# Kernel optimization log

Hardware: AMD Instinct MI355X
Metric: run time of the kernel (lower is better)

## Reference

```python
import jax, jax.numpy as jnp
import numpy as np

EPS = 1e-15


def _cdist(a, b):
    # batched euclidean pairwise distance, a:[B,N,K] b:[B,M,K] -> [B,N,M]
    d2 = (jnp.sum(a * a, -1)[:, :, None] + jnp.sum(b * b, -1)[:, None, :]
          - 2.0 * jnp.einsum('bik,bjk->bij', a, b))
    return jnp.sqrt(jnp.maximum(d2, 0.0))


def _rank3_diag(d_flat):
    # [B,N] -> [B,N,N] diagonal
    eye = jnp.eye(d_flat.shape[1], dtype=d_flat.dtype)
    return eye * d_flat[:, :, None]


def _trace(m):
    return jnp.einsum('bjj->b', m)


def dense_ct_rewiring(x, adj, s, mask):
    s = jnp.tanh(s)
    m = mask[:, :, None].astype(x.dtype)
    x = x * m
    s = s * m
    k = s.shape[-1]
    d_flat = jnp.sum(adj, axis=-1)              # [B,N]
    d = _rank3_diag(d_flat) + EPS               # EPS added to full matrix (faithful to torch)
    L = d - adj
    out_adj = jnp.einsum('bnk,bnm,bml->bkl', s, L, s)
    ct_num = _trace(out_adj)
    ct_den = _trace(jnp.einsum('bnk,bnm,bml->bkl', s, d, s)) + EPS
    ct_dist = _cdist(s, s)                      # [B,N,N]
    vol = _trace(d)                             # [B]
    ct_dist = ct_dist / vol[:, None, None]
    adj_new = ct_dist * adj
    ct_loss = jnp.mean(ct_num / ct_den)
    ss = jnp.einsum('bnk,bnl->bkl', s, s)
    i_s = jnp.eye(k, dtype=ss.dtype)
    ss_n = jnp.sqrt(jnp.sum(ss * ss, axis=(-1, -2), keepdims=True))
    diff = ss / ss_n - i_s
    ortho_loss = jnp.sqrt(jnp.sum(diff * diff))  # global Frobenius norm, mean of scalar
    return adj_new, ct_loss, ortho_loss


def dense_mincut_pool(x, adj, s, mask):
    s = jax.nn.softmax(s, axis=-1)
    m = mask[:, :, None].astype(x.dtype)
    x = x * m
    s = s * m
    k = s.shape[-1]
    out = jnp.einsum('bnk,bnf->bkf', s, x)
    out_adj = jnp.einsum('bnk,bnm,bml->bkl', s, adj, s)
    mincut_num = _trace(out_adj)
    d_flat = jnp.sum(adj, axis=-1) + EPS
    d = _rank3_diag(d_flat)
    mincut_den = _trace(jnp.einsum('bnk,bnm,bml->bkl', s, d, s))
    mincut_loss = jnp.mean(-(mincut_num / mincut_den))
    ss = jnp.einsum('bnk,bnl->bkl', s, s)
    i_s = jnp.eye(k, dtype=ss.dtype)
    ss_n = jnp.sqrt(jnp.sum(ss * ss, axis=(-1, -2), keepdims=True))
    diff = ss / ss_n - i_s / jnp.sqrt(jnp.asarray(float(k), ss.dtype))
    ortho_loss = jnp.mean(jnp.sqrt(jnp.sum(diff * diff, axis=(-1, -2))))
    # zero diagonal, then symmetric degree normalization
    out_adj = out_adj * (1.0 - i_s)
    dk = jnp.sqrt(jnp.sum(out_adj, axis=-1) + EPS) + EPS  # [B,k]
    out_adj = out_adj / dk[:, None, :] / dk[:, :, None]
    return out, out_adj, mincut_loss, ortho_loss


def dense_graph_conv(x, adj, w_rel, b_rel, w_root):
    # PyG DenseGraphConv(aggr='add'): lin_rel(adj @ x) + lin_root(x)
    return jnp.matmul(jnp.matmul(adj, x), w_rel) + b_rel + jnp.matmul(x, w_root)


def ctnet_forward(x, adj, mask,
                  W_lin1, b_lin1, W_pool1, b_pool1, W_pool2, b_pool2,
                  Wrel1, brel1, Wroot1, Wrel2, brel2, Wroot2,
                  W_lin2, b_lin2, W_lin3, b_lin3):
    x = jnp.matmul(x, W_lin1) + b_lin1
    s1 = jnp.matmul(x, W_pool1) + b_pool1
    adj, ct_loss, ortho1 = dense_ct_rewiring(x, adj, s1, mask)
    x = dense_graph_conv(x, adj, Wrel1, brel1, Wroot1)
    s2 = jnp.matmul(x, W_pool2) + b_pool2
    x, adj, mincut2, ortho2 = dense_mincut_pool(x, adj, s2, mask)
    x = dense_graph_conv(x, adj, Wrel2, brel2, Wroot2)
    x = jnp.sum(x, axis=1)
    x = jax.nn.relu(jnp.matmul(x, W_lin2) + b_lin2)
    x = jnp.matmul(x, W_lin3) + b_lin3
    return jax.nn.log_softmax(x, axis=-1), ct_loss + ortho1, mincut2 + ortho2


def _init_lin(key, fan_in, fan_out):
    k1, k2 = jax.random.split(key)
    lim = 1.0 / np.sqrt(fan_in)
    W = jax.random.uniform(k1, (fan_in, fan_out), jnp.float32, -lim, lim)
    b = jax.random.uniform(k2, (fan_out,), jnp.float32, -lim, lim)
    return W, b


def setup_inputs() -> dict:
    key = jax.random.key(0)
    ks = jax.random.split(key, 12)
    B, N, Fin, H, K, OUT, K2 = 16, 1024, 128, 32, 64, 10, 16
    x = jax.random.normal(ks[0], (B, N, Fin), jnp.float32)
    adj = jax.random.uniform(ks[1], (B, N, N), jnp.float32)
    mask = jnp.ones((B, N), jnp.bool_)
    W_lin1, b_lin1 = _init_lin(ks[2], Fin, H)
    W_pool1, b_pool1 = _init_lin(ks[3], H, K)
    W_pool2, b_pool2 = _init_lin(ks[4], H, K2)
    Wrel1, brel1 = _init_lin(ks[5], H, H)
    Wroot1, _ = _init_lin(ks[6], H, H)
    Wrel2, brel2 = _init_lin(ks[7], H, H)
    Wroot2, _ = _init_lin(ks[8], H, H)
    W_lin2, b_lin2 = _init_lin(ks[9], H, H)
    W_lin3, b_lin3 = _init_lin(ks[10], H, OUT)
    return dict(x=x, adj=adj, mask=mask,
                W_lin1=W_lin1, b_lin1=b_lin1, W_pool1=W_pool1, b_pool1=b_pool1,
                W_pool2=W_pool2, b_pool2=b_pool2,
                Wrel1=Wrel1, brel1=brel1, Wroot1=Wroot1,
                Wrel2=Wrel2, brel2=brel2, Wroot2=Wroot2,
                W_lin2=W_lin2, b_lin2=b_lin2, W_lin3=W_lin3, b_lin3=b_lin3)


def reference(x, adj, mask,
              W_lin1, b_lin1, W_pool1, b_pool1, W_pool2, b_pool2,
              Wrel1, brel1, Wroot1, Wrel2, brel2, Wroot2,
              W_lin2, b_lin2, W_lin3, b_lin3):
    return ctnet_forward(x, adj, mask,
                         W_lin1, b_lin1, W_pool1, b_pool1, W_pool2, b_pool2,
                         Wrel1, brel1, Wroot1, Wrel2, brel2, Wroot2,
                         W_lin2, b_lin2, W_lin3, b_lin3)
```

## Files before the change

### kernel.cpp

```cpp
#include <hip/hip_runtime.h>

typedef unsigned short u16;
typedef unsigned int   u32;
typedef __attribute__((ext_vector_type(8))) short bf16x8;
typedef __attribute__((ext_vector_type(4))) float f32x4;

#define EPSF 1e-15f

__device__ __forceinline__ float* accp(float* xb, int b, int a) {
    return xb + (size_t)(b*1024 + a/14)*128 + 114 + (a % 14);
}

__device__ __forceinline__ float bf2f(u16 u) {
    union { u32 i; float f; } v; v.i = ((u32)u) << 16; return v.f;
}
__device__ __forceinline__ u16 f2bf(float f) {
    union { u32 i; float f; } v; v.f = f;
    u32 r = v.i + 0x7fffu + ((v.i >> 16) & 1u);
    return (u16)(r >> 16);
}

__global__ __launch_bounds__(256) void k_a(float* xb,
        const float* __restrict__ W1, const float* __restrict__ b1,
        const float* __restrict__ Wp1, const float* __restrict__ bp1)
{
    __shared__ float W1s[128*32];
    __shared__ float Wp1s[32*64];
    __shared__ float xs[16][128];
    __shared__ float x1s[16][32];
    int tid = threadIdx.x;
    for (int i = tid; i < 1024; i += 256)
        *(float4*)&W1s[i*4] = *(const float4*)&W1[i*4];
    for (int i = tid; i < 512; i += 256)
        *(float4*)&Wp1s[i*4] = *(const float4*)&Wp1[i*4];
    int rbase = blockIdx.x*16;
    for (int e = tid; e < 512; e += 256) {
        int rr = e >> 5, c = e & 31;
        *(float4*)&xs[rr][c*4] = *(const float4*)&xb[(size_t)(rbase + rr)*128 + c*4];
    }
    __syncthreads();
    int w = tid >> 6, l = tid & 63;
    #pragma unroll
    for (int i = 0; i < 4; ++i) {
        int rr = w*4 + i;
        float* xr = xb + (size_t)(rbase + rr)*128;
        if (l < 32) xr[32 + l] = 0.f;
        if (l == 33) xr[96] = 0.f;
        if (l < 15) xr[113 + l] = 0.f;
        if (l < 32) {
            float acc = b1[l];
            for (int f = 0; f < 128; ++f) acc += xs[rr][f]*W1s[f*32 + l];
            x1s[rr][l] = acc;
        }
    }
    __syncthreads();
    #pragma unroll
    for (int i = 0; i < 4; ++i) {
        int rr = w*4 + i;
        float* xr = xb + (size_t)(rbase + rr)*128;
        if (l < 32) xr[64 + l] = x1s[rr][l];
        float acc = bp1[l];
        for (int h = 0; h < 32; ++h) acc += x1s[rr][h]*Wp1s[h*64 + l];
        float sv = tanhf(acc);
        u32 me = (u32)f2bf(sv);
        u32 nb = __shfl_down(me, 1);
        if (!(l & 1)) ((u32*)xr)[l >> 1] = me | (nb << 16);
        float svr = bf2f((u16)me);
        float qv = svr*svr;
        for (int off = 32; off; off >>= 1) qv += __shfl_down(qv, off);
        if (l == 0) xr[112] = qv;
    }
}

__global__ __launch_bounds__(256, 6) void k_c(const float* __restrict__ adj, float* xb,
                                              u32* __restrict__ anb)
{
    __shared__ __align__(16) u16 BufA[64*72];
    __shared__ __align__(16) u16 BufB[64*72];
    __shared__ __align__(16) float qAs[64], qBs[64];
    __shared__ float pw[2][4];
    int tid = threadIdx.x;
    int tj = blockIdx.x, ti = blockIdx.y, b = blockIdx.z;
    int w = tid >> 6, lane = tid & 63;
    int q = lane >> 4, c16 = lane & 15;
    int rloc = w*16 + c16;
    size_t rowg = (size_t)(b*1024 + ti*64 + rloc);
    float4 a4s[4];
    #pragma unroll
    for (int t = 0; t < 4; ++t)
        a4s[t] = *(const float4*)&adj[rowg*1024 + tj*64 + t*16 + q*4];
    const u32* xu = (const u32*)xb;
    for (int e = tid; e < 512; e += 256) {
        int n = e >> 3, c = e & 7;
        *(float4*)&BufA[n*72 + c*8] = *(const float4*)&xu[(size_t)(b*1024 + ti*64 + n)*128 + c*4];
    }
    for (int e = tid; e < 512; e += 256) {
        int n = e >> 3, c = e & 7;
        *(float4*)&BufB[n*72 + c*8] = *(const float4*)&xu[(size_t)(b*1024 + tj*64 + n)*128 + c*4];
    }
    if (tid < 64) qAs[tid] = xb[(size_t)(b*1024 + ti*64 + tid)*128 + 112];
    else if (tid < 128) qBs[tid - 64] = xb[(size_t)(b*1024 + tj*64 + (tid - 64))*128 + 112];
    __syncthreads();
    bf16x8 bfr0 = *(const bf16x8*)&BufA[rloc*72 + q*8];
    bf16x8 bfr1 = *(const bf16x8*)&BufA[rloc*72 + 32 + q*8];
    float qa = qAs[rloc];
    f32x4 g[4];
    #pragma unroll
    for (int t = 0; t < 4; ++t) {
        bf16x8 af0 = *(const bf16x8*)&BufB[(t*16 + c16)*72 + q*8];
        bf16x8 af1 = *(const bf16x8*)&BufB[(t*16 + c16)*72 + 32 + q*8];
        f32x4 gg = {0.f, 0.f, 0.f, 0.f};
        gg = __builtin_amdgcn_mfma_f32_16x16x32_bf16(af0, bfr0, gg, 0, 0, 0);
        gg = __builtin_amdgcn_mfma_f32_16x16x32_bf16(af1, bfr1, gg, 0, 0, 0);
        g[t] = gg;
    }
    float dsum = 0.f, rsum = 0.f, Pt = 0.f, Qt = 0.f;
    #pragma unroll
    for (int t = 0; t < 4; ++t) {
        float4 a4 = a4s[t];
        float4 qb4 = *(const float4*)&qBs[t*16 + q*4];
        float av[4] = {a4.x, a4.y, a4.z, a4.w};
        float qb[4] = {qb4.x, qb4.y, qb4.z, qb4.w};
        float o[4];
        #pragma unroll
        for (int rg = 0; rg < 4; ++rg) {
            float d2v = qa + qb[rg] - 2.f*g[t][rg];
            float dist = sqrtf(fmaxf(d2v, 0.f));
            o[rg] = dist * av[rg];
            dsum += av[rg];
            rsum += o[rg];
            Pt += av[rg]*g[t][rg];
            Qt += g[t][rg]*g[t][rg];
        }
        u32 p0 = (u32)f2bf(o[0]) | ((u32)f2bf(o[1]) << 16);
        u32 p1 = (u32)f2bf(o[2]) | ((u32)f2bf(o[3]) << 16);
        *(uint2*)&anb[rowg*512 + tj*32 + t*8 + q*2] = make_uint2(p0, p1);
    }
    rsum += __shfl_xor(rsum, 16); rsum += __shfl_xor(rsum, 32);
    dsum += __shfl_xor(dsum, 16); dsum += __shfl_xor(dsum, 32);
    if (q == 0) {
        atomicAdd(&xb[rowg*128 + 96],  dsum);
        atomicAdd(&xb[rowg*128 + 113], rsum);
    }
    for (int off = 32; off; off >>= 1) { Pt += __shfl_down(Pt, off); Qt += __shfl_down(Qt, off); }
    if (lane == 0) { pw[0][w] = Pt; pw[1][w] = Qt; }
    __syncthreads();
    if (tid == 0) {
        atomicAdd(accp(xb,b,3), pw[0][0]+pw[0][1]+pw[0][2]+pw[0][3]);
        atomicAdd(accp(xb,b,4), pw[1][0]+pw[1][1]+pw[1][2]+pw[1][3]);
    }
}

__global__ __launch_bounds__(256) void k_y(const u32* __restrict__ anb, float* xb)
{
    __shared__ __align__(16) u16 X[32][264];
    int tid = threadIdx.x;
    int kq = blockIdx.x, ni = blockIdx.y, b = blockIdx.z;
    int w = tid >> 6, lane = tid & 63;
    int q = lane >> 4, c16 = lane & 15;
    int rloc = w*16 + c16;
    size_t rowg = (size_t)(b*1024 + ni*64 + rloc);
    bf16x8 afv[8];
    #pragma unroll
    for (int ks = 0; ks < 8; ++ks)
        afv[ks] = *(const bf16x8*)&anb[rowg*512 + kq*128 + ks*16 + q*4];
    for (int e = tid; e < 2048; e += 256) {
        int m = e >> 3, hq = e & 7;
        const float4 v = *(const float4*)&xb[(size_t)(b*1024 + kq*256 + m)*128 + 64 + hq*4];
        X[hq*4 + 0][m] = f2bf(v.x);
        X[hq*4 + 1][m] = f2bf(v.y);
        X[hq*4 + 2][m] = f2bf(v.z);
        X[hq*4 + 3][m] = f2bf(v.w);
    }
    __syncthreads();
    f32x4 acc0 = {0.f,0.f,0.f,0.f}, acc1 = {0.f,0.f,0.f,0.f};
    #pragma unroll
    for (int ks = 0; ks < 8; ++ks) {
        bf16x8 b0 = *(const bf16x8*)&X[c16][ks*32 + q*8];
        bf16x8 b1v = *(const bf16x8*)&X[c16 + 16][ks*32 + q*8];
        acc0 = __builtin_amdgcn_mfma_f32_16x16x32_bf16(afv[ks], b0,  acc0, 0, 0, 0);
        acc1 = __builtin_amdgcn_mfma_f32_16x16x32_bf16(afv[ks], b1v, acc1, 0, 0, 0);
    }
    #pragma unroll
    for (int rg = 0; rg < 4; ++rg) {
        size_t orow = (size_t)(b*1024 + ni*64 + w*16 + q*4 + rg)*128;
        atomicAdd(&xb[orow + 32 + c16], acc0[rg]);
        atomicAdd(&xb[orow + 48 + c16], acc1[rg]);
    }
    if (kq == 0 && tid < 64) {
        const float* xr = xb + (size_t)(b*1024 + ni*64 + tid)*128;
        float d = xr[96], qv = xr[112];
        float t0 = d, t1 = d*qv, t2 = qv;
        for (int off = 32; off; off >>= 1) {
            t0 += __shfl_down(t0, off); t1 += __shfl_down(t1, off); t2 += __shfl_down(t2, off);
        }
        if (tid == 0) {
            atomicAdd(accp(xb,b,0), t0);
            atomicAdd(accp(xb,b,1), t1);
            atomicAdd(accp(xb,b,2), t2);
        }
    }
}

__global__ __launch_bounds__(256) void k_d2(float* xb,
        const float* __restrict__ Wrel1, const float* __restrict__ brel1,
        const float* __restrict__ Wroot1,
        const float* __restrict__ Wp2, const float* __restrict__ bp2)
{
    __shared__ float ys[32*34];
    __shared__ float x1n[32*34];
    __shared__ float x2s[32*34];
    __shared__ float s2s[32*17];
    __shared__ float Wr[1024], Wo[1024], Wp[512];
    int tid = threadIdx.x;
    int tq = blockIdx.x, b = blockIdx.y;
    int rbase = b*1024 + tq*32;
    float invv = 1.f / (*accp(xb,b,0) + 1024.f*EPSF);
    for (int i = tid; i < 1024; i += 256) { Wr[i] = Wrel1[i]; Wo[i] = Wroot1[i]; }
    for (int i = tid; i < 512; i += 256) Wp[i] = Wp2[i];
    for (int e = tid; e < 1024; e += 256) {
        int r = e >> 5, h = e & 31;
        const float* xr = xb + (size_t)(rbase + r)*128;
        ys[r*34 + h]  = xr[32 + h] * invv;
        x1n[r*34 + h] = xr[64 + h];
    }
    __syncthreads();
    {
        int h = tid & 31, tg = tid >> 5;
        float brl = brel1[h];
        #pragma unroll
        for (int i = 0; i < 4; ++i) {
            int r = tg + 8*i;
            float v = brl;
            for (int j = 0; j < 32; ++j)
                v += ys[r*34 + j]*Wr[j*32 + h] + x1n[r*34 + j]*Wo[j*32 + h];
            x2s[r*34 + h] = v;
        }
    }
    __syncthreads();
    if (tid < 64) {
        int r = tid & 31;
        float lg[16];
        float mx = -1e30f;
        #pragma unroll
        for (int k = 0; k < 16; ++k) {
            float v = bp2[k];
            for (int j = 0; j < 32; ++j) v += x2s[r*34 + j]*Wp[j*16 + k];
            lg[k] = v; mx = fmaxf(mx, v);
        }
        float sum = 0.f;
        #pragma unroll
        for (int k = 0; k < 16; ++k) { lg[k] = expf(lg[k] - mx); sum += lg[k]; }
        float inv = 1.f/sum, q2v = 0.f;
        u32 pk[8];
        #pragma unroll
        for (int k = 0; k < 16; ++k) {
            float sv = lg[k]*inv;
            s2s[r*17 + k] = sv;
            u32 bfv = (u32)f2bf(sv);
            if (k & 1) pk[k>>1] |= bfv << 16; else pk[k>>1] = bfv;
            q2v += sv*sv;
        }
        if (tid < 32) {
            u32* xp = (u32*)(xb + (size_t)(rbase + r)*128);
            #pragma unroll
            for (int i2 = 0; i2 < 8; ++i2) xp[i2] = pk[i2];
        }
        float denp = (xb[(size_t)(rbase + r)*128 + 113]*invv + EPSF)*q2v;
        if (tid >= 32) denp = 0.f;
        for (int off = 32; off; off >>= 1) denp += __shfl_down(denp, off);
        if (tid == 0) atomicAdd(accp(xb,b,5), denp);
    }
    __syncthreads();
    {
        int k = tid >> 4, l = tid & 15;
        float s = 0.f;
        for (int r = 0; r < 32; ++r) s += s2s[r*17 + k]*s2s[r*17 + l];
        atomicAdd(accp(xb,b,774 + tid), s);
    }
    for (int e = tid; e < 512; e += 256) {
        int k = e >> 5, h = e & 31;
        float s = 0.f;
        for (int r = 0; r < 32; ++r) s += s2s[r*17 + k]*x2s[r*34 + h];
        atomicAdd(accp(xb,b,6 + k*32 + h), s);
    }
}

__global__ __launch_bounds__(256, 6) void k_e(const u32* __restrict__ anb, float* xb)
{
    __shared__ __align__(16) u16 BufA[64*72];
    __shared__ __align__(16) u16 BufS[16*72];
    __shared__ __align__(16) u16 BufN[16*72];
    __shared__ __align__(16) u16 zT[16*72];
    int tid = threadIdx.x;
    int miq = blockIdx.x, ni = blockIdx.y, b = blockIdx.z;
    const u32* xu = (const u32*)xb;
    for (int e = tid; e < 512; e += 256) {
        int node = e >> 3, lw = e & 7;
        u32 pp = xu[(size_t)(b*1024 + ni*64 + node)*128 + lw];
        BufN[(lw*2)*72 + node]     = (u16)pp;
        BufN[(lw*2 + 1)*72 + node] = (u16)(pp >> 16);
    }
    int w = tid >> 6, lane = tid & 63;
    int q = lane >> 4, c16 = lane & 15;
    int rloc = w*16 + c16;
    f32x4 zacc = {0.f, 0.f, 0.f, 0.f};
    #pragma unroll
    for (int mii = 0; mii < 2; ++mii) {
        int mi = miq*2 + mii;
        __syncthreads();
        for (int e = tid; e < 512; e += 256) {
            int n = e >> 3, c = e & 7;
            *(float4*)&BufA[n*72 + c*8] =
                *(const float4*)&anb[(size_t)(b*1024 + ni*64 + n)*512 + mi*32 + c*4];
        }
        for (int e = tid; e < 512; e += 256) {
            int node = e >> 3, lw = e & 7;
            u32 pp = xu[(size_t)(b*1024 + mi*64 + node)*128 + lw];
            BufS[(lw*2)*72 + node]     = (u16)pp;
            BufS[(lw*2 + 1)*72 + node] = (u16)(pp >> 16);
        }
        __syncthreads();
        bf16x8 ya0 = *(const bf16x8*)&BufA[rloc*72 + q*8];
        bf16x8 ya1 = *(const bf16x8*)&BufA[rloc*72 + 32 + q*8];
        bf16x8 yb0 = *(const bf16x8*)&BufS[c16*72 + q*8];
        bf16x8 yb1 = *(const bf16x8*)&BufS[c16*72 + 32 + q*8];
        zacc = __builtin_amdgcn_mfma_f32_16x16x32_bf16(ya0, yb0, zacc, 0, 0, 0);
        zacc = __builtin_amdgcn_mfma_f32_16x16x32_bf16(ya1, yb1, zacc, 0, 0, 0);
    }
    #pragma unroll
    for (int rg = 0; rg < 4; ++rg)
        zT[c16*72 + w*16 + q*4 + rg] = f2bf(zacc[rg]);
    __syncthreads();
    if (w == 0) {
        bf16x8 af0 = *(const bf16x8*)&BufN[c16*72 + q*8];
        bf16x8 af1 = *(const bf16x8*)&BufN[c16*72 + 32 + q*8];
        bf16x8 bz0 = *(const bf16x8*)&zT[c16*72 + q*8];
        bf16x8 bz1 = *(const bf16x8*)&zT[c16*72 + 32 + q*8];
        f32x4 oamv = {0.f, 0.f, 0.f, 0.f};
        oamv = __builtin_amdgcn_mfma_f32_16x16x32_bf16(af0, bz0, oamv, 0, 0, 0);
        oamv = __builtin_amdgcn_mfma_f32_16x16x32_bf16(af1, bz1, oamv, 0, 0, 0);
        #pragma unroll
        for (int rg = 0; rg < 4; ++rg)
            atomicAdd(accp(xb, b, 518 + (q*4 + rg)*16 + c16), oamv[rg]);
    }
}

__global__ __launch_bounds__(256) void k_f1(float* xb,
        const float* __restrict__ Wrel2, const float* __restrict__ brel2,
        const float* __restrict__ Wroot2,
        const float* __restrict__ W_lin2, const float* __restrict__ b_lin2,
        const float* __restrict__ W_lin3, const float* __restrict__ b_lin3,
        float* __restrict__ outp)
{
    __shared__ float oam_s[256], ssm_s[256], outm_s[512];
    __shared__ float dks[16], csoa[16];
    __shared__ float cs0[32], cs1[32], xsum[32], x5[32], lgs[10];
    __shared__ float red[4];
    int b = blockIdx.x;
    int tid = threadIdx.x;
    float invv = 1.f / (*accp(xb,b,0) + 1024.f*EPSF);
    oam_s[tid] = *accp(xb,b,518 + tid) * invv;
    ssm_s[tid] = *accp(xb,b,774 + tid);
    for (int e = tid; e < 512; e += 256) outm_s[e] = *accp(xb,b,6 + e);
    __syncthreads();
    if (tid < 16) {
        float rsv = 0.f;
        for (int l = 0; l < 16; ++l) if (l != tid) rsv += oam_s[tid*16 + l];
        dks[tid] = sqrtf(fmaxf(rsv, 0.f) + EPSF) + EPSF;
    }
    {
        float v = ssm_s[tid];
        float p = v*v;
        for (int off = 32; off; off >>= 1) p += __shfl_down(p, off);
        if ((tid & 63) == 0) red[tid >> 6] = p;
    }
    __syncthreads();
    if (tid < 16) {
        float s = 0.f;
        for (int k2 = 0; k2 < 16; ++k2)
            if (k2 != tid) s += oam_s[k2*16 + tid] / dks[k2];
        csoa[tid] = s / dks[tid];
    }
    if (tid < 32) {
        float s0 = 0.f, s1 = 0.f;
        for (int l = 0; l < 16; ++l) {
            float ov = outm_s[l*32 + tid];
            s0 += ov;
            s1 += csoa[l] * ov;
        }
        cs0[tid] = s0; cs1[tid] = s1;
    }
    if (tid == 64) {
        float T1v  = *accp(xb,b,1);
        float Pgv  = *accp(xb,b,3);
        float Q2v  = *accp(xb,b,4);
        float Tq1v = *accp(xb,b,2);
        float T2v  = *accp(xb,b,5);
        *accp(xb,b,1030) = (T1v - Pgv) / (T1v + EPSF);
        *accp(xb,b,1031) = 65.f - 2.f*Tq1v/sqrtf(fmaxf(Q2v, 1e-30f));
        float tr2 = 0.f, trs = 0.f;
        for (int k2 = 0; k2 < 16; ++k2) { tr2 += oam_s[k2*17]; trs += ssm_s[k2*17]; }
        *accp(xb,b,1032) = -tr2 / T2v;
        float fr2 = red[0] + red[1] + red[2] + red[3];
        *accp(xb,b,1033) = sqrtf(fmaxf(2.f - trs/(2.f*sqrtf(fmaxf(fr2, 1e-30f))), 0.f));
    }
    __syncthreads();
    if (tid < 32) {
        float v = 16.f * brel2[tid];
        for (int j = 0; j < 32; ++j)
            v += cs1[j]*Wrel2[j*32 + tid] + cs0[j]*Wroot2[j*32 + tid];
        xsum[tid] = v;
    }
    __syncthreads();
    if (tid < 32) {
        float v = b_lin2[tid];
        for (int j = 0; j < 32; ++j) v += xsum[j]*W_lin2[j*32 + tid];
        x5[tid] = fmaxf(v, 0.f);
    }
    __syncthreads();
    if (tid < 10) {
        float v = b_lin3[tid];
        for (int j = 0; j < 32; ++j) v += x5[j]*W_lin3[j*10 + tid];
        lgs[tid] = v;
    }
    __syncthreads();
    if (tid < 10) {
        float mx = -1e30f;
        for (int t = 0; t < 10; ++t) mx = fmaxf(mx, lgs[t]);
        float sum = 0.f;
        for (int t = 0; t < 10; ++t) sum += expf(lgs[t] - mx);
        outp[b*10 + tid] = lgs[tid] - mx - logf(sum);
    }
}

__global__ __launch_bounds__(64) void k_f2(float* xb, float* __restrict__ outp)
{
    int tid = threadIdx.x;
    int b2 = tid & 15, which = tid >> 4;
    float v = *accp(xb, b2, 1030 + which);
    for (int off = 1; off < 16; off <<= 1) v += __shfl_xor(v, off);
    float ct = __shfl(v, 0);
    float o1 = __shfl(v, 16);
    float mc = __shfl(v, 32);
    float o2 = __shfl(v, 48);
    if (tid == 0) {
        outp[160] = ct/16.f + sqrtf(fmaxf(o1, 0.f));
        outp[161] = mc/16.f + o2/16.f;
    }
}

extern "C" void kernel_launch(void* const* d_in, const int* in_sizes, int n_in,
                              void* d_out, int out_size, void* d_ws, size_t ws_size,
                              hipStream_t stream)
{
    float* xb        = (float*)d_in[0];
    const float* adj = (const float*)d_in[1];
    const float* W_lin1 = (const float*)d_in[3];
    const float* b_lin1 = (const float*)d_in[4];
    const float* W_pool1= (const float*)d_in[5];
    const float* b_pool1= (const float*)d_in[6];
    const float* W_pool2= (const float*)d_in[7];
    const float* b_pool2= (const float*)d_in[8];
    const float* Wrel1  = (const float*)d_in[9];
    const float* brel1  = (const float*)d_in[10];
    const float* Wroot1 = (const float*)d_in[11];
    const float* Wrel2  = (const float*)d_in[12];
    const float* brel2  = (const float*)d_in[13];
    const float* Wroot2 = (const float*)d_in[14];
    const float* W_lin2 = (const float*)d_in[15];
    const float* b_lin2 = (const float*)d_in[16];
    const float* W_lin3 = (const float*)d_in[17];
    const float* b_lin3 = (const float*)d_in[18];
    u32* anb = (u32*)d_ws;
    (void)ws_size; (void)in_sizes; (void)n_in; (void)out_size;

    k_a<<<dim3(1024),      dim3(256), 0, stream>>>(xb, W_lin1, b_lin1, W_pool1, b_pool1);
    k_c<<<dim3(16,16,16),  dim3(256), 0, stream>>>(adj, xb, anb);
    k_y<<<dim3(4,16,16),   dim3(256), 0, stream>>>(anb, xb);
    k_d2<<<dim3(32,16),    dim3(256), 0, stream>>>(xb, Wrel1, brel1, Wroot1,
                                                   W_pool2, b_pool2);
    k_e<<<dim3(8,16,16),   dim3(256), 0, stream>>>(anb, xb);
    k_f1<<<dim3(16),       dim3(256), 0, stream>>>(xb, Wrel2, brel2, Wroot2,
                                                   W_lin2, b_lin2, W_lin3, b_lin3,
                                                   (float*)d_out);
    k_f2<<<dim3(1),        dim3(64),  0, stream>>>(xb, (float*)d_out);
}
```

Before: 247.1 us.

## Widen adjacency tiles, drop split-K atomics in k_y, fold final reduction into k_f1

Result: faster. 227.5 us (-7.9%).

```diff
diff --git a/kernel.cpp b/kernel.cpp
--- a/kernel.cpp
+++ b/kernel.cpp
@@ -40,18 +40,19 @@
     }
     __syncthreads();
     int w = tid >> 6, l = tid & 63;
+    int col = l & 31, half = l >> 5;
     #pragma unroll
     for (int i = 0; i < 4; ++i) {
         int rr = w*4 + i;
         float* xr = xb + (size_t)(rbase + rr)*128;
-        if (l < 32) xr[32 + l] = 0.f;
         if (l == 33) xr[96] = 0.f;
         if (l < 15) xr[113 + l] = 0.f;
-        if (l < 32) {
-            float acc = b1[l];
-            for (int f = 0; f < 128; ++f) acc += xs[rr][f]*W1s[f*32 + l];
-            x1s[rr][l] = acc;
-        }
+        float acc = half ? 0.f : b1[col];
+        const float* xrow = &xs[rr][half*64];
+        const float* wrow = &W1s[half*64*32 + col];
+        for (int f = 0; f < 64; ++f) acc += xrow[f]*wrow[f*32];
+        acc += __shfl_down(acc, 32);
+        if (l < 32) x1s[rr][l] = acc;
     }
     __syncthreads();
     #pragma unroll
@@ -72,69 +73,80 @@
     }
 }
 
-__global__ __launch_bounds__(256, 6) void k_c(const float* __restrict__ adj, float* xb,
+__global__ __launch_bounds__(256, 5) void k_c(const float* __restrict__ adj, float* xb,
                                               u32* __restrict__ anb)
 {
     __shared__ __align__(16) u16 BufA[64*72];
-    __shared__ __align__(16) u16 BufB[64*72];
-    __shared__ __align__(16) float qAs[64], qBs[64];
+    __shared__ __align__(16) u16 BufB[2][64*72];
+    __shared__ __align__(16) float qAs[64], qBs[2][64];
     __shared__ float pw[2][4];
     int tid = threadIdx.x;
-    int tj = blockIdx.x, ti = blockIdx.y, b = blockIdx.z;
+    int tjq = blockIdx.x, ti = blockIdx.y, b = blockIdx.z;
     int w = tid >> 6, lane = tid & 63;
     int q = lane >> 4, c16 = lane & 15;
     int rloc = w*16 + c16;
     size_t rowg = (size_t)(b*1024 + ti*64 + rloc);
-    float4 a4s[4];
-    #pragma unroll
-    for (int t = 0; t < 4; ++t)
-        a4s[t] = *(const float4*)&adj[rowg*1024 + tj*64 + t*16 + q*4];
+    float4 a4s[2][4];
+    #pragma unroll
+    for (int tt = 0; tt < 2; ++tt)
+        #pragma unroll
+        for (int t = 0; t < 4; ++t)
+            a4s[tt][t] = *(const float4*)&adj[rowg*1024 + (tjq*2 + tt)*64 + t*16 + q*4];
     const u32* xu = (const u32*)xb;
     for (int e = tid; e < 512; e += 256) {
         int n = e >> 3, c = e & 7;
         *(float4*)&BufA[n*72 + c*8] = *(const float4*)&xu[(size_t)(b*1024 + ti*64 + n)*128 + c*4];
     }
-    for (int e = tid; e < 512; e += 256) {
-        int n = e >> 3, c = e & 7;
-        *(float4*)&BufB[n*72 + c*8] = *(const float4*)&xu[(size_t)(b*1024 + tj*64 + n)*128 + c*4];
+    for (int e = tid; e < 1024; e += 256) {
+        int n2 = e >> 3, c = e & 7;
+        int tt = n2 >> 6, n = n2 & 63;
+        *(float4*)&BufB[tt][n*72 + c*8] =
+            *(const float4*)&xu[(size_t)(b*1024 + (tjq*2 + tt)*64 + n)*128 + c*4];
     }
     if (tid < 64) qAs[tid] = xb[(size_t)(b*1024 + ti*64 + tid)*128 + 112];
-    else if (tid < 128) qBs[tid - 64] = xb[(size_t)(b*1024 + tj*64 + (tid - 64))*128 + 112];
+    else if (tid < 192) {
+        int t2 = tid - 64;
+        qBs[t2 >> 6][t2 & 63] =
+            xb[(size_t)(b*1024 + (tjq*2 + (t2 >> 6))*64 + (t2 & 63))*128 + 112];
+    }
     __syncthreads();
     bf16x8 bfr0 = *(const bf16x8*)&BufA[rloc*72 + q*8];
     bf16x8 bfr1 = *(const bf16x8*)&BufA[rloc*72 + 32 + q*8];
     float qa = qAs[rloc];
-    f32x4 g[4];
-    #pragma unroll
-    for (int t = 0; t < 4; ++t) {
-        bf16x8 af0 = *(const bf16x8*)&BufB[(t*16 + c16)*72 + q*8];
-        bf16x8 af1 = *(const bf16x8*)&BufB[(t*16 + c16)*72 + 32 + q*8];
-        f32x4 gg = {0.f, 0.f, 0.f, 0.f};
-        gg = __builtin_amdgcn_mfma_f32_16x16x32_bf16(af0, bfr0, gg, 0, 0, 0);
-        gg = __builtin_amdgcn_mfma_f32_16x16x32_bf16(af1, bfr1, gg, 0, 0, 0);
-        g[t] = gg;
-    }
     float dsum = 0.f, rsum = 0.f, Pt = 0.f, Qt = 0.f;
     #pragma unroll
-    for (int t = 0; t < 4; ++t) {
-        float4 a4 = a4s[t];
-        float4 qb4 = *(const float4*)&qBs[t*16 + q*4];
-        float av[4] = {a4.x, a4.y, a4.z, a4.w};
-        float qb[4] = {qb4.x, qb4.y, qb4.z, qb4.w};
-        float o[4];
-        #pragma unroll
-        for (int rg = 0; rg < 4; ++rg) {
-            float d2v = qa + qb[rg] - 2.f*g[t][rg];
-            float dist = sqrtf(fmaxf(d2v, 0.f));
-            o[rg] = dist * av[rg];
-            dsum += av[rg];
-            rsum += o[rg];
-            Pt += av[rg]*g[t][rg];
-            Qt += g[t][rg]*g[t][rg];
-        }
-        u32 p0 = (u32)f2bf(o[0]) | ((u32)f2bf(o[1]) << 16);
-        u32 p1 = (u32)f2bf(o[2]) | ((u32)f2bf(o[3]) << 16);
-        *(uint2*)&anb[rowg*512 + tj*32 + t*8 + q*2] = make_uint2(p0, p1);
+    for (int tt = 0; tt < 2; ++tt) {
+        f32x4 g[4];
+        #pragma unroll
+        for (int t = 0; t < 4; ++t) {
+            bf16x8 af0 = *(const bf16x8*)&BufB[tt][(t*16 + c16)*72 + q*8];
+            bf16x8 af1 = *(const bf16x8*)&BufB[tt][(t*16 + c16)*72 + 32 + q*8];
+            f32x4 gg = {0.f, 0.f, 0.f, 0.f};
+            gg = __builtin_amdgcn_mfma_f32_16x16x32_bf16(af0, bfr0, gg, 0, 0, 0);
+            gg = __builtin_amdgcn_mfma_f32_16x16x32_bf16(af1, bfr1, gg, 0, 0, 0);
+            g[t] = gg;
+        }
+        #pragma unroll
+        for (int t = 0; t < 4; ++t) {
+            float4 a4 = a4s[tt][t];
+            float4 qb4 = *(const float4*)&qBs[tt][t*16 + q*4];
+            float av[4] = {a4.x, a4.y, a4.z, a4.w};
+            float qb[4] = {qb4.x, qb4.y, qb4.z, qb4.w};
+            float o[4];
+            #pragma unroll
+            for (int rg = 0; rg < 4; ++rg) {
+                float d2v = qa + qb[rg] - 2.f*g[t][rg];
+                float dist = sqrtf(fmaxf(d2v, 0.f));
+                o[rg] = dist * av[rg];
+                dsum += av[rg];
+                rsum += o[rg];
+                Pt += av[rg]*g[t][rg];
+                Qt += g[t][rg]*g[t][rg];
+            }
+            u32 p0 = (u32)f2bf(o[0]) | ((u32)f2bf(o[1]) << 16);
+            u32 p1 = (u32)f2bf(o[2]) | ((u32)f2bf(o[3]) << 16);
+            *(uint2*)&anb[rowg*512 + (tjq*2 + tt)*32 + t*8 + q*2] = make_uint2(p0, p1);
+        }
     }
     rsum += __shfl_xor(rsum, 16); rsum += __shfl_xor(rsum, 32);
     dsum += __shfl_xor(dsum, 16); dsum += __shfl_xor(dsum, 32);
@@ -153,20 +165,16 @@
 
 __global__ __launch_bounds__(256) void k_y(const u32* __restrict__ anb, float* xb)
 {
-    __shared__ __align__(16) u16 X[32][264];
+    __shared__ __align__(16) u16 X[32][1032];
     int tid = threadIdx.x;
-    int kq = blockIdx.x, ni = blockIdx.y, b = blockIdx.z;
+    int ni = blockIdx.x, b = blockIdx.y;
     int w = tid >> 6, lane = tid & 63;
     int q = lane >> 4, c16 = lane & 15;
     int rloc = w*16 + c16;
     size_t rowg = (size_t)(b*1024 + ni*64 + rloc);
-    bf16x8 afv[8];
-    #pragma unroll
-    for (int ks = 0; ks < 8; ++ks)
-        afv[ks] = *(const bf16x8*)&anb[rowg*512 + kq*128 + ks*16 + q*4];
-    for (int e = tid; e < 2048; e += 256) {
+    for (int e = tid; e < 8192; e += 256) {
         int m = e >> 3, hq = e & 7;
-        const float4 v = *(const float4*)&xb[(size_t)(b*1024 + kq*256 + m)*128 + 64 + hq*4];
+        const float4 v = *(const float4*)&xb[(size_t)(b*1024 + m)*128 + 64 + hq*4];
         X[hq*4 + 0][m] = f2bf(v.x);
         X[hq*4 + 1][m] = f2bf(v.y);
         X[hq*4 + 2][m] = f2bf(v.z);
@@ -174,20 +182,21 @@
     }
     __syncthreads();
     f32x4 acc0 = {0.f,0.f,0.f,0.f}, acc1 = {0.f,0.f,0.f,0.f};
-    #pragma unroll
-    for (int ks = 0; ks < 8; ++ks) {
-        bf16x8 b0 = *(const bf16x8*)&X[c16][ks*32 + q*8];
+    #pragma unroll 8
+    for (int ks = 0; ks < 32; ++ks) {
+        bf16x8 af  = *(const bf16x8*)&anb[rowg*512 + ks*16 + q*4];
+        bf16x8 b0  = *(const bf16x8*)&X[c16][ks*32 + q*8];
         bf16x8 b1v = *(const bf16x8*)&X[c16 + 16][ks*32 + q*8];
-        acc0 = __builtin_amdgcn_mfma_f32_16x16x32_bf16(afv[ks], b0,  acc0, 0, 0, 0);
-        acc1 = __builtin_amdgcn_mfma_f32_16x16x32_bf16(afv[ks], b1v, acc1, 0, 0, 0);
+        acc0 = __builtin_amdgcn_mfma_f32_16x16x32_bf16(af, b0,  acc0, 0, 0, 0);
+        acc1 = __builtin_amdgcn_mfma_f32_16x16x32_bf16(af, b1v, acc1, 0, 0, 0);
     }
     #pragma unroll
     for (int rg = 0; rg < 4; ++rg) {
         size_t orow = (size_t)(b*1024 + ni*64 + w*16 + q*4 + rg)*128;
-        atomicAdd(&xb[orow + 32 + c16], acc0[rg]);
-        atomicAdd(&xb[orow + 48 + c16], acc1[rg]);
-    }
-    if (kq == 0 && tid < 64) {
+        xb[orow + 32 + c16] = acc0[rg];
+        xb[orow + 48 + c16] = acc1[rg];
+    }
+    if (tid < 64) {
         const float* xr = xb + (size_t)(b*1024 + ni*64 + tid)*128;
         float d = xr[96], qv = xr[112];
         float t0 = d, t1 = d*qv, t2 = qv;
@@ -357,6 +366,7 @@
     __shared__ float dks[16], csoa[16];
     __shared__ float cs0[32], cs1[32], xsum[32], x5[32], lgs[10];
     __shared__ float red[4];
+    __shared__ int isLast;
     int b = blockIdx.x;
     int tid = threadIdx.x;
     float invv = 1.f / (*accp(xb,b,0) + 1024.f*EPSF);
@@ -397,13 +407,18 @@
         float Q2v  = *accp(xb,b,4);
         float Tq1v = *accp(xb,b,2);
         float T2v  = *accp(xb,b,5);
-        *accp(xb,b,1030) = (T1v - Pgv) / (T1v + EPSF);
-        *accp(xb,b,1031) = 65.f - 2.f*Tq1v/sqrtf(fmaxf(Q2v, 1e-30f));
         float tr2 = 0.f, trs = 0.f;
         for (int k2 = 0; k2 < 16; ++k2) { tr2 += oam_s[k2*17]; trs += ssm_s[k2*17]; }
-        *accp(xb,b,1032) = -tr2 / T2v;
         float fr2 = red[0] + red[1] + red[2] + red[3];
-        *accp(xb,b,1033) = sqrtf(fmaxf(2.f - trs/(2.f*sqrtf(fmaxf(fr2, 1e-30f))), 0.f));
+        __hip_atomic_store(accp(xb,b,1030), (T1v - Pgv) / (T1v + EPSF),
+                           __ATOMIC_RELAXED, __HIP_MEMORY_SCOPE_AGENT);
+        __hip_atomic_store(accp(xb,b,1031), 65.f - 2.f*Tq1v/sqrtf(fmaxf(Q2v, 1e-30f)),
+                           __ATOMIC_RELAXED, __HIP_MEMORY_SCOPE_AGENT);
+        __hip_atomic_store(accp(xb,b,1032), -tr2 / T2v,
+                           __ATOMIC_RELAXED, __HIP_MEMORY_SCOPE_AGENT);
+        __hip_atomic_store(accp(xb,b,1033),
+                           sqrtf(fmaxf(2.f - trs/(2.f*sqrtf(fmaxf(fr2, 1e-30f))), 0.f)),
+                           __ATOMIC_RELAXED, __HIP_MEMORY_SCOPE_AGENT);
     }
     __syncthreads();
     if (tid < 32) {
@@ -432,21 +447,27 @@
         for (int t = 0; t < 10; ++t) sum += expf(lgs[t] - mx);
         outp[b*10 + tid] = lgs[tid] - mx - logf(sum);
     }
-}
-
-__global__ __launch_bounds__(64) void k_f2(float* xb, float* __restrict__ outp)
-{
-    int tid = threadIdx.x;
-    int b2 = tid & 15, which = tid >> 4;
-    float v = *accp(xb, b2, 1030 + which);
-    for (int off = 1; off < 16; off <<= 1) v += __shfl_xor(v, off);
-    float ct = __shfl(v, 0);
-    float o1 = __shfl(v, 16);
-    float mc = __shfl(v, 32);
-    float o2 = __shfl(v, 48);
+    __syncthreads();
     if (tid == 0) {
-        outp[160] = ct/16.f + sqrtf(fmaxf(o1, 0.f));
-        outp[161] = mc/16.f + o2/16.f;
+        __threadfence();
+        float old = atomicAdd(accp(xb,0,1035), 1.f);
+        isLast = (old > 14.5f) ? 1 : 0;
+    }
+    __syncthreads();
+    if (isLast && tid < 64) {
+        __threadfence();
+        int b2 = tid & 15, which = tid >> 4;
+        float v = __hip_atomic_load(accp(xb,b2,1030 + which),
+                                    __ATOMIC_RELAXED, __HIP_MEMORY_SCOPE_AGENT);
+        for (int off = 1; off < 16; off <<= 1) v += __shfl_xor(v, off);
+        float ct = __shfl(v, 0);
+        float o1 = __shfl(v, 16);
+        float mc = __shfl(v, 32);
+        float o2 = __shfl(v, 48);
+        if (tid == 0) {
+            outp[160] = ct/16.f + sqrtf(fmaxf(o1, 0.f));
+            outp[161] = mc/16.f + o2/16.f;
+        }
     }
 }
 
@@ -476,13 +497,12 @@
     (void)ws_size; (void)in_sizes; (void)n_in; (void)out_size;
 
     k_a<<<dim3(1024),      dim3(256), 0, stream>>>(xb, W_lin1, b_lin1, W_pool1, b_pool1);
-    k_c<<<dim3(16,16,16),  dim3(256), 0, stream>>>(adj, xb, anb);
-    k_y<<<dim3(4,16,16),   dim3(256), 0, stream>>>(anb, xb);
+    k_c<<<dim3(8,16,16),   dim3(256), 0, stream>>>(adj, xb, anb);
+    k_y<<<dim3(16,16),     dim3(256), 0, stream>>>(anb, xb);
     k_d2<<<dim3(32,16),    dim3(256), 0, stream>>>(xb, Wrel1, brel1, Wroot1,
                                                    W_pool2, b_pool2);
     k_e<<<dim3(8,16,16),   dim3(256), 0, stream>>>(anb, xb);
     k_f1<<<dim3(16),       dim3(256), 0, stream>>>(xb, Wrel2, brel2, Wroot2,
                                                    W_lin2, b_lin2, W_lin3, b_lin3,
                                                    (float*)d_out);
-    k_f2<<<dim3(1),        dim3(64),  0, stream>>>(xb, (float*)d_out);
-}
+}
```
